# Optimization experiments

Measured on AMD Instinct MI355X. Metric: run time of the kernel, lower is better.

Reference implementation:

```python
import jax, jax.numpy as jnp
import numpy as np

D_MODEL = 1024
D_FF = 4096
NUM_EXPERTS = 8
TOP_K = 2
CAPACITY_FACTOR = 1.25


def setup_inputs() -> dict:
    key = jax.random.key(0)
    ks = jax.random.split(key, 5)
    scale_d = 1.0 / np.sqrt(D_MODEL)
    scale_f = 1.0 / np.sqrt(D_FF)
    x = jax.random.normal(ks[0], (4, 2048, D_MODEL), dtype=jnp.float32)
    gate_w = jax.random.uniform(ks[1], (NUM_EXPERTS, D_MODEL), jnp.float32, -scale_d, scale_d)
    w1 = jax.random.uniform(ks[2], (NUM_EXPERTS, D_FF, D_MODEL), jnp.float32, -scale_d, scale_d)
    w3 = jax.random.uniform(ks[3], (NUM_EXPERTS, D_FF, D_MODEL), jnp.float32, -scale_d, scale_d)
    w2 = jax.random.uniform(ks[4], (NUM_EXPERTS, D_MODEL, D_FF), jnp.float32, -scale_f, scale_f)
    return {"x": x, "gate_w": gate_w, "w1": w1, "w2": w2, "w3": w3}


def reference(x, gate_w, w1, w2, w3):
    B, S, D = x.shape
    E = gate_w.shape[0]
    xf = x.reshape(-1, D)                       # [N, D]
    N = xf.shape[0]
    capacity = int(N / E * CAPACITY_FACTOR)

    # ---- Router ----
    router_logits = xf @ gate_w.T               # [N, E]
    router_probs = jax.nn.softmax(router_logits, axis=-1)
    top_probs, top_idx = jax.lax.top_k(router_probs, TOP_K)   # [N, K]
    top_w = top_probs / (top_probs.sum(-1, keepdims=True) + 1e-10)

    erange = jnp.arange(E, dtype=top_idx.dtype)
    out = jnp.zeros_like(xf)
    for k in range(TOP_K):
        idx = top_idx[:, k]                     # [N]
        # rank of each token within its expert's queue (original token order)
        onehot = (idx[:, None] == erange[None, :]).astype(jnp.int32)  # [N, E]
        pos_all = jnp.cumsum(onehot, axis=0) - 1                       # [N, E]
        pos = jnp.take_along_axis(pos_all, idx[:, None], axis=1)[:, 0]  # [N]
        keep = pos < capacity                    # capacity truncation (keep first `capacity` tokens)
        slot = jnp.clip(pos, 0, capacity - 1)

        # dispatch: [E, capacity, D]
        buf = jnp.zeros((E, capacity, D), xf.dtype)
        buf = buf.at[idx, slot].add(jnp.where(keep[:, None], xf, 0.0))

        # grouped SwiGLU FFN per expert
        h = jax.nn.silu(jnp.einsum('ecd,efd->ecf', buf, w1)) * jnp.einsum('ecd,efd->ecf', buf, w3)
        ob = jnp.einsum('ecf,edf->ecd', h, w2)   # [E, capacity, D]

        # combine back to token order with routing weights
        gathered = ob[idx, slot]                 # [N, D]
        out = out + gathered * (keep.astype(xf.dtype) * top_w[:, k])[:, None]

    output = out.reshape(B, S, D)

    # ---- load-balance aux loss (Switch formulation) ----
    counts = jnp.sum((top_idx[..., None] == erange[None, None, :]).astype(jnp.float32), axis=(0, 1))  # [E]
    f = counts / (N * TOP_K)
    P = router_probs.mean(axis=0)
    aux_loss = E * jnp.sum(f * P)
    return output, aux_loss
```

## Files before the change

### kernel.cpp

```cpp
#include <hip/hip_runtime.h>
#include <stdint.h>

#define D_MODEL 1024
#define D_FF    4096
#define NE      8
#define NTOK    8192
#define CAP     1280
#define RPE     2560
#define RTOT    (NE*RPE)
#define TM      128
#define TN1     64
#define TN      128
#define BK      64
#define RBLK    (NTOK/4)

typedef __attribute__((ext_vector_type(8))) short s8v;
typedef __attribute__((ext_vector_type(4))) float f4v;

__device__ inline unsigned short f2bf(float f) {
    unsigned int u = __float_as_uint(f);
    u += 0x7fffu + ((u >> 16) & 1u);
    return (unsigned short)(u >> 16);
}

__device__ __forceinline__ void gload16(const unsigned short* g, unsigned short* l) {
    __builtin_amdgcn_global_load_lds(
        (const __attribute__((address_space(1))) unsigned int*)g,
        (__attribute__((address_space(3))) unsigned int*)l,
        16, 0, 0);
}

__global__ __launch_bounds__(256) void cvt_kernel(const float* __restrict__ src,
                                                  unsigned short* __restrict__ dst, int n4) {
    int i = blockIdx.x * blockDim.x + threadIdx.x;
    int stride = gridDim.x * blockDim.x;
    for (; i < n4; i += stride) {
        float4 v = ((const float4*)src)[i];
        union { unsigned short us[4]; uint2 u2; } cv;
        cv.us[0] = f2bf(v.x); cv.us[1] = f2bf(v.y);
        cv.us[2] = f2bf(v.z); cv.us[3] = f2bf(v.w);
        ((uint2*)dst)[i] = cv.u2;
    }
}

__global__ __launch_bounds__(256) void router_kernel(const float* __restrict__ x,
                                                     const float* __restrict__ gate,
                                                     int* __restrict__ e0a, int* __restrict__ e1a,
                                                     float* __restrict__ w0a, float* __restrict__ w1a,
                                                     float* __restrict__ partial) {
    __shared__ float gs[NE * D_MODEL];
    __shared__ float ps[NE];
    int tid = threadIdx.x;
    for (int i = tid; i < NE * D_MODEL; i += 256) gs[i] = gate[i];
    if (tid < NE) ps[tid] = 0.0f;
    __syncthreads();
    int wv = tid >> 6, lane = tid & 63;
    int t = blockIdx.x * 4 + wv;
    const float* xr = x + (size_t)t * D_MODEL;
    double acc[NE];
    #pragma unroll
    for (int e = 0; e < NE; e++) acc[e] = 0.0;
    #pragma unroll
    for (int j = 0; j < 16; j++) {
        int d = lane + 64 * j;
        double xv = (double)xr[d];
        #pragma unroll
        for (int e = 0; e < NE; e++) acc[e] += xv * (double)gs[e * D_MODEL + d];
    }
    #pragma unroll
    for (int e = 0; e < NE; e++) {
        #pragma unroll
        for (int off = 32; off > 0; off >>= 1) acc[e] += __shfl_xor(acc[e], off);
    }
    if (lane == 0) {
        double mx = acc[0];
        #pragma unroll
        for (int e = 1; e < NE; e++) mx = fmax(mx, acc[e]);
        double p[NE], s = 0.0;
        #pragma unroll
        for (int e = 0; e < NE; e++) { p[e] = exp(acc[e] - mx); s += p[e]; }
        float p32[NE];
        #pragma unroll
        for (int e = 0; e < NE; e++) p32[e] = (float)(p[e] / s);
        int b0 = 0;
        #pragma unroll
        for (int e = 1; e < NE; e++) if (p32[e] > p32[b0]) b0 = e;
        int b1 = (b0 == 0) ? 1 : 0;
        #pragma unroll
        for (int e = 0; e < NE; e++) if (e != b0 && p32[e] > p32[b1]) b1 = e;
        float denom = p32[b0] + p32[b1] + 1e-10f;
        e0a[t] = b0; e1a[t] = b1;
        w0a[t] = p32[b0] / denom;
        w1a[t] = p32[b1] / denom;
        #pragma unroll
        for (int e = 0; e < NE; e++) atomicAdd(&ps[e], p32[e]);
    }
    __syncthreads();
    if (tid < NE) partial[blockIdx.x * NE + tid] = ps[tid];
}

__global__ __launch_bounds__(512) void scan_kernel(const int* __restrict__ e0a, const int* __restrict__ e1a,
                                                   const float* __restrict__ w0a, const float* __restrict__ w1a,
                                                   int* __restrict__ tok, float* __restrict__ wl,
                                                   int* __restrict__ M, int* __restrict__ counts) {
    int e = threadIdx.x >> 6;
    int lane = threadIdx.x & 63;
    unsigned long long below = (1ull << lane) - 1ull;
    int c = 0;
    for (int base = 0; base < NTOK; base += 64) {
        int t = base + lane;
        bool m = (e0a[t] == e);
        unsigned long long mask = __ballot(m);
        int pos = c + __popcll(mask & below);
        if (m && pos < CAP) { tok[e * RPE + pos] = t; wl[e * RPE + pos] = w0a[t]; }
        c += __popcll(mask);
    }
    int c0 = c;
    int base0 = (c0 < CAP) ? c0 : CAP;
    c = 0;
    for (int base = 0; base < NTOK; base += 64) {
        int t = base + lane;
        bool m = (e1a[t] == e);
        unsigned long long mask = __ballot(m);
        int pos = c + __popcll(mask & below);
        if (m && pos < CAP) { tok[e * RPE + base0 + pos] = t; wl[e * RPE + base0 + pos] = w1a[t]; }
        c += __popcll(mask);
    }
    int c1 = c;
    if (lane == 0) {
        M[e] = base0 + ((c1 < CAP) ? c1 : CAP);
        counts[e] = c0 + c1;
    }
}

__global__ __launch_bounds__(256) void gather_kernel(const float* __restrict__ x,
                                                     const int* __restrict__ tok,
                                                     const int* __restrict__ M,
                                                     unsigned short* __restrict__ Xg) {
    int wv = threadIdx.x >> 6, lane = threadIdx.x & 63;
    int r = blockIdx.x * 4 + wv;
    int e = r / RPE;
    int i = r - e * RPE;
    unsigned short* dst = Xg + (size_t)r * D_MODEL;
    if (i < M[e]) {
        int t = tok[r];
        const float4* src = (const float4*)(x + (size_t)t * D_MODEL);
        #pragma unroll
        for (int j = 0; j < 4; j++) {
            float4 v = src[lane + 64 * j];
            union { unsigned short us[4]; uint2 u2; } cv;
            cv.us[0] = f2bf(v.x); cv.us[1] = f2bf(v.y);
            cv.us[2] = f2bf(v.z); cv.us[3] = f2bf(v.w);
            *(uint2*)(dst + (size_t)(lane + 64 * j) * 4) = cv.u2;
        }
    } else {
        uint2 z; z.x = 0u; z.y = 0u;
        #pragma unroll
        for (int j = 0; j < 4; j++) *(uint2*)(dst + (size_t)(lane + 64 * j) * 4) = z;
    }
}

__global__ __launch_bounds__(256, 2) void gemm1_kernel(const unsigned short* __restrict__ Xg,
                                                       const unsigned short* __restrict__ Wb1,
                                                       const unsigned short* __restrict__ Wb3,
                                                       const int* __restrict__ M,
                                                       unsigned short* __restrict__ H) {
    __shared__ __align__(16) unsigned short As[TM * BK];
    __shared__ __align__(16) unsigned short B1s[TN1 * BK];
    __shared__ __align__(16) unsigned short B3s[TN1 * BK];
    int bx = blockIdx.x;
    int e = bx / 1280;
    int r = bx - e * 1280;
    int nt = r / 20;
    int mt = r - nt * 20;
    if (mt * TM >= M[e]) return;
    const unsigned short* Ab  = Xg  + ((size_t)e * RPE + (size_t)mt * TM) * D_MODEL;
    const unsigned short* B1b = Wb1 + (size_t)e * D_FF * D_MODEL + (size_t)nt * TN1 * D_MODEL;
    const unsigned short* B3b = Wb3 + (size_t)e * D_FF * D_MODEL + (size_t)nt * TN1 * D_MODEL;
    int tid = threadIdx.x;
    int lane = tid & 63, wv = tid >> 6;
    int wm = wv & 1, wn = wv >> 1;
    int quad = lane >> 4, l16 = lane & 15;
    f4v acc1[4][2], acc3[4][2];
    #pragma unroll
    for (int i = 0; i < 4; i++)
        #pragma unroll
        for (int j = 0; j < 2; j++) { acc1[i][j] = 0.0f; acc3[i][j] = 0.0f; }

    for (int kt = 0; kt < D_MODEL / BK; kt++) {
        int kof = kt * BK;
        __syncthreads();
        #pragma unroll
        for (int c = 0; c < 4; c++) {
            int chunk = c * 256 + tid;
            int row = chunk >> 3;
            int ch  = chunk & 7;
            int gcol = (ch ^ (row & 7)) * 8;
            int lb = (c * 256 + wv * 64) * 8;
            gload16(Ab + (size_t)row * D_MODEL + kof + gcol, As + lb);
        }
        #pragma unroll
        for (int c = 0; c < 2; c++) {
            int chunk = c * 256 + tid;
            int row = chunk >> 3;
            int ch  = chunk & 7;
            int gcol = (ch ^ (row & 7)) * 8;
            int lb = (c * 256 + wv * 64) * 8;
            gload16(B1b + (size_t)row * D_MODEL + kof + gcol, B1s + lb);
            gload16(B3b + (size_t)row * D_MODEL + kof + gcol, B3s + lb);
        }
        __syncthreads();
        #pragma unroll
        for (int st = 0; st < 2; st++) {
            s8v af[4], bf1[2], bf3[2];
            int cbase = st * 32 + quad * 8;
            #pragma unroll
            for (int i = 0; i < 4; i++) {
                int row = wm * 64 + i * 16 + l16;
                af[i] = *(const s8v*)(As + row * BK + (cbase ^ ((row & 7) << 3)));
            }
            #pragma unroll
            for (int j = 0; j < 2; j++) {
                int row = wn * 32 + j * 16 + l16;
                bf1[j] = *(const s8v*)(B1s + row * BK + (cbase ^ ((row & 7) << 3)));
                bf3[j] = *(const s8v*)(B3s + row * BK + (cbase ^ ((row & 7) << 3)));
            }
            #pragma unroll
            for (int i = 0; i < 4; i++)
                #pragma unroll
                for (int j = 0; j < 2; j++) {
                    acc1[i][j] = __builtin_amdgcn_mfma_f32_16x16x32_bf16(af[i], bf1[j], acc1[i][j], 0, 0, 0);
                    acc3[i][j] = __builtin_amdgcn_mfma_f32_16x16x32_bf16(af[i], bf3[j], acc3[i][j], 0, 0, 0);
                }
        }
    }
    size_t rowbase = (size_t)e * RPE + (size_t)mt * TM;
    #pragma unroll
    for (int i = 0; i < 4; i++) {
        #pragma unroll
        for (int j = 0; j < 2; j++) {
            int col = nt * TN1 + wn * 32 + j * 16 + l16;
            #pragma unroll
            for (int rg = 0; rg < 4; rg++) {
                int row = wm * 64 + i * 16 + quad * 4 + rg;
                float z = acc1[i][j][rg];
                float sg = z / (1.0f + __expf(-z));
                float h = sg * acc3[i][j][rg];
                H[(rowbase + row) * (size_t)D_FF + col] = f2bf(h);
            }
        }
    }
}

__global__ __launch_bounds__(256, 2) void gemm2_kernel(const unsigned short* __restrict__ H,
                                                       const unsigned short* __restrict__ Wb2,
                                                       const int* __restrict__ tok,
                                                       const float* __restrict__ wl,
                                                       const int* __restrict__ M,
                                                       float* __restrict__ out) {
    __shared__ __align__(16) unsigned short As[TM * BK];
    __shared__ __align__(16) unsigned short Bs[TN * BK];
    __shared__ int   tok_s[TM];
    __shared__ float wl_s[TM];
    int bx = blockIdx.x;
    int e = bx / 160;
    int r = bx - e * 160;
    int mt = r >> 3;
    int nt = r & 7;
    int Me = M[e];
    if (mt * TM >= Me) return;
    const unsigned short* Ab = H + ((size_t)e * RPE + (size_t)mt * TM) * D_FF;
    const unsigned short* Bb = Wb2 + (size_t)e * D_MODEL * D_FF + (size_t)nt * TN * D_FF;
    int tid = threadIdx.x;
    if (tid < TM) {
        tok_s[tid] = tok[e * RPE + mt * TM + tid];
        wl_s[tid]  = wl[e * RPE + mt * TM + tid];
    }
    int lane = tid & 63, wv = tid >> 6;
    int wm = wv & 1, wn = wv >> 1;
    int quad = lane >> 4, l16 = lane & 15;
    f4v acc[4][4];
    #pragma unroll
    for (int i = 0; i < 4; i++)
        #pragma unroll
        for (int j = 0; j < 4; j++) acc[i][j] = 0.0f;

    for (int kt = 0; kt < D_FF / BK; kt++) {
        int kof = kt * BK;
        __syncthreads();
        #pragma unroll
        for (int c = 0; c < 4; c++) {
            int chunk = c * 256 + tid;
            int row = chunk >> 3;
            int ch  = chunk & 7;
            int gcol = (ch ^ (row & 7)) * 8;
            int lb = (c * 256 + wv * 64) * 8;
            gload16(Ab + (size_t)row * D_FF + kof + gcol, As + lb);
            gload16(Bb + (size_t)row * D_FF + kof + gcol, Bs + lb);
        }
        __syncthreads();
        #pragma unroll
        for (int st = 0; st < 2; st++) {
            s8v af[4], bf[4];
            int cbase = st * 32 + quad * 8;
            #pragma unroll
            for (int i = 0; i < 4; i++) {
                int row = wm * 64 + i * 16 + l16;
                af[i] = *(const s8v*)(As + row * BK + (cbase ^ ((row & 7) << 3)));
            }
            #pragma unroll
            for (int j = 0; j < 4; j++) {
                int row = wn * 64 + j * 16 + l16;
                bf[j] = *(const s8v*)(Bs + row * BK + (cbase ^ ((row & 7) << 3)));
            }
            #pragma unroll
            for (int i = 0; i < 4; i++)
                #pragma unroll
                for (int j = 0; j < 4; j++)
                    acc[i][j] = __builtin_amdgcn_mfma_f32_16x16x32_bf16(af[i], bf[j], acc[i][j], 0, 0, 0);
        }
    }
    int mbase = mt * TM;
    #pragma unroll
    for (int i = 0; i < 4; i++) {
        #pragma unroll
        for (int j = 0; j < 4; j++) {
            int col = nt * TN + wn * 64 + j * 16 + l16;
            #pragma unroll
            for (int rg = 0; rg < 4; rg++) {
                int row = wm * 64 + i * 16 + quad * 4 + rg;
                if (mbase + row < Me) {
                    float v = acc[i][j][rg] * wl_s[row];
                    atomicAdd(out + (size_t)tok_s[row] * D_MODEL + col, v);
                }
            }
        }
    }
}

__global__ __launch_bounds__(64) void aux_kernel(const int* __restrict__ counts,
                                                 const float* __restrict__ partial,
                                                 float* __restrict__ out_aux) {
    __shared__ float red[64];
    int tid = threadIdx.x;
    int e = tid & 7;
    int chunk = tid >> 3;
    float s = 0.0f;
    for (int b = chunk * (RBLK / 8); b < (chunk + 1) * (RBLK / 8); b++)
        s += partial[b * NE + e];
    red[tid] = s;
    __syncthreads();
    if (tid == 0) {
        float total = 0.0f;
        for (int e2 = 0; e2 < NE; e2++) {
            float P = 0.0f;
            for (int c = 0; c < 8; c++) P += red[c * 8 + e2];
            P /= (float)NTOK;
            float f = (float)counts[e2] / (float)(NTOK * 2);
            total += f * P;
        }
        *out_aux = (float)NE * total;
    }
}

extern "C" void kernel_launch(void* const* d_in, const int* in_sizes, int n_in,
                              void* d_out, int out_size, void* d_ws, size_t ws_size,
                              hipStream_t stream) {
    (void)in_sizes; (void)n_in; (void)ws_size;
    const float* x    = (const float*)d_in[0];
    const float* gate = (const float*)d_in[1];
    const float* w1   = (const float*)d_in[2];
    const float* w2   = (const float*)d_in[3];
    const float* w3   = (const float*)d_in[4];
    float* out = (float*)d_out;

    const size_t WB = (size_t)NE * D_FF * D_MODEL * 2;
    char* p = (char*)d_ws;
    unsigned short* Wb1 = (unsigned short*)p;  p += WB;
    unsigned short* Wb3 = (unsigned short*)p;  p += WB;
    unsigned short* Wb2 = (unsigned short*)p;  p += WB;
    unsigned short* Xg  = (unsigned short*)p;  p += (size_t)RTOT * D_MODEL * 2;
    unsigned short* H   = (unsigned short*)p;  p += (size_t)RTOT * D_FF * 2;
    int*   e0a = (int*)p;    p += NTOK * 4;
    int*   e1a = (int*)p;    p += NTOK * 4;
    float* w0a = (float*)p;  p += NTOK * 4;
    float* w1a = (float*)p;  p += NTOK * 4;
    int*   tok = (int*)p;    p += RTOT * 4;
    float* wl  = (float*)p;  p += RTOT * 4;
    int*   M   = (int*)p;    p += 64;
    int*   counts = (int*)p; p += 64;
    float* partial = (float*)p; p += RBLK * NE * 4;

    hipMemsetAsync(d_out, 0, (size_t)out_size * 4, stream);

    int n4 = NE * D_FF * D_MODEL / 4;
    cvt_kernel<<<2048, 256, 0, stream>>>(w1, Wb1, n4);
    cvt_kernel<<<2048, 256, 0, stream>>>(w3, Wb3, n4);
    cvt_kernel<<<2048, 256, 0, stream>>>(w2, Wb2, n4);

    router_kernel<<<RBLK, 256, 0, stream>>>(x, gate, e0a, e1a, w0a, w1a, partial);
    scan_kernel<<<1, 512, 0, stream>>>(e0a, e1a, w0a, w1a, tok, wl, M, counts);
    gather_kernel<<<RTOT / 4, 256, 0, stream>>>(x, tok, M, Xg);

    gemm1_kernel<<<NE * 20 * 64, 256, 0, stream>>>(Xg, Wb1, Wb3, M, H);
    gemm2_kernel<<<NE * 20 * 8, 256, 0, stream>>>(H, Wb2, tok, wl, M, out);

    aux_kernel<<<1, 64, 0, stream>>>(counts, partial, out + (size_t)NTOK * D_MODEL);
}
```

Before: 1.124 ms.

## Replace atomic scatter-add combine with dense expert output plus inverse-index combine kernel

gemm2 now writes its per-slot expert outputs densely into a scratch buffer that reuses the Wb1 region, instead of doing weighted atomicAdds into the token output. The scan kernel records, for each token, the slot it landed in for each of its two experts (-1 if dropped), and a new combine kernel gathers both rows and applies the routing weights. This removes the output memset and the float atomics. It also adds a full write and read pass over the expert outputs. Both GEMM grids also remap block indices so that blocks from different experts interleave across the launch order.

```diff
diff --git a/kernel.cpp b/kernel.cpp
--- a/kernel.cpp
+++ b/kernel.cpp
@@ -100,8 +100,8 @@
 }
 
 __global__ __launch_bounds__(512) void scan_kernel(const int* __restrict__ e0a, const int* __restrict__ e1a,
-                                                   const float* __restrict__ w0a, const float* __restrict__ w1a,
-                                                   int* __restrict__ tok, float* __restrict__ wl,
+                                                   int* __restrict__ tok,
+                                                   int* __restrict__ inv0, int* __restrict__ inv1,
                                                    int* __restrict__ M, int* __restrict__ counts) {
     int e = threadIdx.x >> 6;
     int lane = threadIdx.x & 63;
@@ -112,7 +112,10 @@
         bool m = (e0a[t] == e);
         unsigned long long mask = __ballot(m);
         int pos = c + __popcll(mask & below);
-        if (m && pos < CAP) { tok[e * RPE + pos] = t; wl[e * RPE + pos] = w0a[t]; }
+        if (m) {
+            if (pos < CAP) { tok[e * RPE + pos] = t; inv0[t] = e * RPE + pos; }
+            else inv0[t] = -1;
+        }
         c += __popcll(mask);
     }
     int c0 = c;
@@ -123,7 +126,10 @@
         bool m = (e1a[t] == e);
         unsigned long long mask = __ballot(m);
         int pos = c + __popcll(mask & below);
-        if (m && pos < CAP) { tok[e * RPE + base0 + pos] = t; wl[e * RPE + base0 + pos] = w1a[t]; }
+        if (m) {
+            if (pos < CAP) { tok[e * RPE + base0 + pos] = t; inv1[t] = e * RPE + base0 + pos; }
+            else inv1[t] = -1;
+        }
         c += __popcll(mask);
     }
     int c1 = c;
@@ -168,7 +174,7 @@
     __shared__ __align__(16) unsigned short As[TM * BK];
     __shared__ __align__(16) unsigned short B1s[TN1 * BK];
     __shared__ __align__(16) unsigned short B3s[TN1 * BK];
-    int bx = blockIdx.x;
+    int bx = (blockIdx.x & 7) * (NE * 1280 / 8) + (blockIdx.x >> 3);
     int e = bx / 1280;
     int r = bx - e * 1280;
     int nt = r / 20;
@@ -254,28 +260,19 @@
 
 __global__ __launch_bounds__(256, 2) void gemm2_kernel(const unsigned short* __restrict__ H,
                                                        const unsigned short* __restrict__ Wb2,
-                                                       const int* __restrict__ tok,
-                                                       const float* __restrict__ wl,
                                                        const int* __restrict__ M,
-                                                       float* __restrict__ out) {
+                                                       float* __restrict__ O) {
     __shared__ __align__(16) unsigned short As[TM * BK];
     __shared__ __align__(16) unsigned short Bs[TN * BK];
-    __shared__ int   tok_s[TM];
-    __shared__ float wl_s[TM];
-    int bx = blockIdx.x;
+    int bx = (blockIdx.x & 7) * (NE * 160 / 8) + (blockIdx.x >> 3);
     int e = bx / 160;
     int r = bx - e * 160;
     int mt = r >> 3;
     int nt = r & 7;
-    int Me = M[e];
-    if (mt * TM >= Me) return;
+    if (mt * TM >= M[e]) return;
     const unsigned short* Ab = H + ((size_t)e * RPE + (size_t)mt * TM) * D_FF;
     const unsigned short* Bb = Wb2 + (size_t)e * D_MODEL * D_FF + (size_t)nt * TN * D_FF;
     int tid = threadIdx.x;
-    if (tid < TM) {
-        tok_s[tid] = tok[e * RPE + mt * TM + tid];
-        wl_s[tid]  = wl[e * RPE + mt * TM + tid];
-    }
     int lane = tid & 63, wv = tid >> 6;
     int wm = wv & 1, wn = wv >> 1;
     int quad = lane >> 4, l16 = lane & 15;
@@ -320,7 +317,7 @@
                     acc[i][j] = __builtin_amdgcn_mfma_f32_16x16x32_bf16(af[i], bf[j], acc[i][j], 0, 0, 0);
         }
     }
-    int mbase = mt * TM;
+    size_t rowbase = (size_t)e * RPE + (size_t)mt * TM;
     #pragma unroll
     for (int i = 0; i < 4; i++) {
         #pragma unroll
@@ -329,12 +326,37 @@
             #pragma unroll
             for (int rg = 0; rg < 4; rg++) {
                 int row = wm * 64 + i * 16 + quad * 4 + rg;
-                if (mbase + row < Me) {
-                    float v = acc[i][j][rg] * wl_s[row];
-                    atomicAdd(out + (size_t)tok_s[row] * D_MODEL + col, v);
-                }
-            }
-        }
+                O[(rowbase + row) * (size_t)D_MODEL + col] = acc[i][j][rg];
+            }
+        }
+    }
+}
+
+__global__ __launch_bounds__(256) void combine_kernel(const float* __restrict__ O,
+                                                      const int* __restrict__ inv0,
+                                                      const int* __restrict__ inv1,
+                                                      const float* __restrict__ w0a,
+                                                      const float* __restrict__ w1a,
+                                                      float* __restrict__ out) {
+    int wv = threadIdx.x >> 6, lane = threadIdx.x & 63;
+    int t = blockIdx.x * 4 + wv;
+    int r0 = inv0[t], r1 = inv1[t];
+    float w0 = w0a[t], w1 = w1a[t];
+    const float4* O0 = (const float4*)(O + (size_t)(r0 < 0 ? 0 : r0) * D_MODEL);
+    const float4* O1 = (const float4*)(O + (size_t)(r1 < 0 ? 0 : r1) * D_MODEL);
+    float4* dst = (float4*)(out + (size_t)t * D_MODEL);
+    float4 z; z.x = z.y = z.z = z.w = 0.0f;
+    #pragma unroll
+    for (int j = 0; j < 4; j++) {
+        int d = lane + 64 * j;
+        float4 a = (r0 >= 0) ? O0[d] : z;
+        float4 b = (r1 >= 0) ? O1[d] : z;
+        float4 rr;
+        rr.x = w0 * a.x + w1 * b.x;
+        rr.y = w0 * a.y + w1 * b.y;
+        rr.z = w0 * a.z + w1 * b.z;
+        rr.w = w0 * a.w + w1 * b.w;
+        dst[d] = rr;
     }
 }
 
@@ -366,7 +388,7 @@
 extern "C" void kernel_launch(void* const* d_in, const int* in_sizes, int n_in,
                               void* d_out, int out_size, void* d_ws, size_t ws_size,
                               hipStream_t stream) {
-    (void)in_sizes; (void)n_in; (void)ws_size;
+    (void)in_sizes; (void)n_in; (void)ws_size; (void)out_size;
     const float* x    = (const float*)d_in[0];
     const float* gate = (const float*)d_in[1];
     const float* w1   = (const float*)d_in[2];
@@ -386,12 +408,13 @@
     float* w0a = (float*)p;  p += NTOK * 4;
     float* w1a = (float*)p;  p += NTOK * 4;
     int*   tok = (int*)p;    p += RTOT * 4;
-    float* wl  = (float*)p;  p += RTOT * 4;
+    int*   inv0 = (int*)p;   p += NTOK * 4;
+    int*   inv1 = (int*)p;   p += NTOK * 4;
     int*   M   = (int*)p;    p += 64;
     int*   counts = (int*)p; p += 64;
     float* partial = (float*)p; p += RBLK * NE * 4;
 
-    hipMemsetAsync(d_out, 0, (size_t)out_size * 4, stream);
+    float* O = (float*)Wb1;
 
     int n4 = NE * D_FF * D_MODEL / 4;
     cvt_kernel<<<2048, 256, 0, stream>>>(w1, Wb1, n4);
@@ -399,11 +422,12 @@
     cvt_kernel<<<2048, 256, 0, stream>>>(w2, Wb2, n4);
 
     router_kernel<<<RBLK, 256, 0, stream>>>(x, gate, e0a, e1a, w0a, w1a, partial);
-    scan_kernel<<<1, 512, 0, stream>>>(e0a, e1a, w0a, w1a, tok, wl, M, counts);
+    scan_kernel<<<1, 512, 0, stream>>>(e0a, e1a, tok, inv0, inv1, M, counts);
     gather_kernel<<<RTOT / 4, 256, 0, stream>>>(x, tok, M, Xg);
 
     gemm1_kernel<<<NE * 20 * 64, 256, 0, stream>>>(Xg, Wb1, Wb3, M, H);
-    gemm2_kernel<<<NE * 20 * 8, 256, 0, stream>>>(H, Wb2, tok, wl, M, out);
-
+    gemm2_kernel<<<NE * 20 * 8, 256, 0, stream>>>(H, Wb2, M, O);
+
+    combine_kernel<<<NTOK / 4, 256, 0, stream>>>(O, inv0, inv1, w0a, w1a, out);
     aux_kernel<<<1, 64, 0, stream>>>(counts, partial, out + (size_t)NTOK * D_MODEL);
 }
```

Result: faster. 1.063 ms (-5.4%).
